# Kernel optimization log

Measured on AMD Instinct MI355X. Metric: run time of the kernel, lower is better.

Reference implementation:

```python
import jax, jax.numpy as jnp
import numpy as np

DIM = 1024
H = 16
D = DIM // H  # 64
EPS = 1e-6


def _rmsnorm(x, scale):
    # per-last-dim RMSNorm, computed in fp32 like the torch code
    rms = jax.lax.rsqrt(jnp.mean(x * x, axis=-1, keepdims=True) + EPS)
    return x * rms * scale


def _apply_rope(xq, xk, pe):
    # xq, xk: [B,H,L,D]; pe: [1,1,L,D/2,2,2]
    B, h, L, d = xq.shape
    xq_ = xq.reshape(B, h, L, d // 2, 1, 2)
    xk_ = xk.reshape(B, h, L, d // 2, 1, 2)
    xq_out = pe[..., 0] * xq_[..., 0] + pe[..., 1] * xq_[..., 1]  # [B,H,L,D/2,2]
    xk_out = pe[..., 0] * xk_[..., 0] + pe[..., 1] * xk_[..., 1]
    return xq_out.reshape(B, h, L, d), xk_out.reshape(B, h, L, d)


def setup_inputs() -> dict:
    key = jax.random.key(0)
    ks = jax.random.split(key, 6)
    B, L = 2, 2048
    x = jax.random.normal(ks[0], (B, L, DIM), dtype=jnp.float32)
    pe = jax.random.normal(ks[1], (1, 1, L, D // 2, 2, 2), dtype=jnp.float32)
    qkv_w = jax.random.normal(ks[2], (3 * DIM, DIM), dtype=jnp.float32) * (DIM ** -0.5)
    q_scale = jnp.ones((D,), dtype=jnp.float32)
    k_scale = jnp.ones((D,), dtype=jnp.float32)
    proj_w = jax.random.normal(ks[3], (DIM, DIM), dtype=jnp.float32) * (DIM ** -0.5)
    proj_b = jnp.zeros((DIM,), dtype=jnp.float32)
    return {"x": x, "pe": pe, "qkv_w": qkv_w, "q_scale": q_scale,
            "k_scale": k_scale, "proj_w": proj_w, "proj_b": proj_b}


def reference(x, pe, qkv_w, q_scale, k_scale, proj_w, proj_b):
    B, L, _ = x.shape
    x_c = jnp.clip(jnp.nan_to_num(x, nan=0.0, posinf=0.0, neginf=0.0), -10000.0, 10000.0)
    qkv = x_c @ qkv_w.T  # [B,L,3*DIM] (qkv_bias=False)
    qkv = jnp.nan_to_num(qkv, nan=0.0, posinf=0.0, neginf=0.0)
    # 'B L (K H D) -> K B H L D'
    qkv = qkv.reshape(B, L, 3, H, D).transpose(2, 0, 3, 1, 4)
    q, k, v = qkv[0], qkv[1], qkv[2]  # each [B,H,L,D]
    q = _rmsnorm(q, q_scale)
    k = _rmsnorm(k, k_scale)
    q, k = _apply_rope(q, k, pe)
    # scaled dot product attention (no mask)
    scores = jnp.einsum('bhqd,bhkd->bhqk', q, k) * (D ** -0.5)
    attn = jax.nn.softmax(scores, axis=-1)
    out = jnp.einsum('bhqk,bhkd->bhqd', attn, v)
    out = out.transpose(0, 2, 1, 3).reshape(B, L, H * D)  # 'B H L D -> B L (H D)'
    out = jnp.clip(out, -10000.0, 10000.0)
    return out @ proj_w.T + proj_b
```

## Files before the change

### kernel.cpp

```cpp
#include <hip/hip_runtime.h>
#include <hip/hip_bf16.h>

#define DIMC 1024
#define HEADS 16
#define HD 64
#define BATCH 2
#define SEQ 2048

typedef __bf16 bf16;
typedef __bf16 bf16x4 __attribute__((ext_vector_type(4)));
typedef __bf16 bf16x8 __attribute__((ext_vector_type(8)));
typedef float f32x4 __attribute__((ext_vector_type(4)));

typedef const __attribute__((address_space(1))) void* gas_t;
typedef __attribute__((address_space(3))) void* las_t;

__device__ inline f32x4 mfma_bf16(bf16x8 a, bf16x8 b, f32x4 c) {
    return __builtin_amdgcn_mfma_f32_16x16x32_bf16(a, b, c, 0, 0, 0);
}

__device__ inline void st8(bf16* p, bf16x8 v) {
    *(bf16x4*)p       = *(bf16x4*)&v;
    *(bf16x4*)(p + 4) = *((bf16x4*)&v + 1);
}
__device__ inline bf16x8 ld_frag(const bf16* p) {
    bf16x8 r;
    *(bf16x4*)&r       = *(const bf16x4*)p;
    *((bf16x4*)&r + 1) = *(const bf16x4*)(p + 16);
    return r;
}
__device__ inline bf16x8 ld_frag_s(const bf16* rowp, int cb, int sw) {
    bf16x8 r;
    *(bf16x4*)&r       = *(const bf16x4*)((const char*)rowp + ((cb) ^ sw));
    *((bf16x4*)&r + 1) = *(const bf16x4*)((const char*)rowp + ((cb + 32) ^ sw));
    return r;
}

__global__ __launch_bounds__(256) void k_prep_x(const float* __restrict__ x,
                                                bf16* __restrict__ xb) {
    int i = blockIdx.x * 256 + threadIdx.x;
    float4 v = ((const float4*)x)[i];
    float a[4] = {v.x, v.y, v.z, v.w};
    bf16x4 o;
#pragma unroll
    for (int j = 0; j < 4; ++j) {
        float f = a[j];
        f = __builtin_isfinite(f) ? fminf(fmaxf(f, -10000.f), 10000.f) : 0.f;
        o[j] = (bf16)f;
    }
    ((bf16x4*)xb)[i] = o;
}

__global__ __launch_bounds__(256) void k_cast(const float* __restrict__ a,
                                              bf16* __restrict__ o) {
    int i = blockIdx.x * 256 + threadIdx.x;
    float4 v = ((const float4*)a)[i];
    bf16x4 r = {(bf16)v.x, (bf16)v.y, (bf16)v.z, (bf16)v.w};
    ((bf16x4*)o)[i] = r;
}

template <bool OUT_BF16, bool BIAS, bool SANITIZE>
__global__ __launch_bounds__(256) void k_gemm_bt(const bf16* __restrict__ A,
                                                 const bf16* __restrict__ Bt,
                                                 void* __restrict__ Cv,
                                                 const float* __restrict__ bias,
                                                 int N, int K) {
    __shared__ alignas(16) bf16 As[128 * 64];
    __shared__ alignas(16) bf16 Bs[128 * 64];
    const int t = threadIdx.x;
    const int m0 = blockIdx.y * 128, n0 = blockIdx.x * 128;
    const int w = t >> 6, lane = t & 63;
    const int wm = (w >> 1) * 64, wn = (w & 1) * 64;
    const int lr = lane & 15, lg = lane >> 4;
    const int srow = lane >> 3;
    const int scol = ((lane & 7) ^ srow) * 8;
    const int sw = (lr & 7) << 4;

    f32x4 acc[4][4];
#pragma unroll
    for (int i = 0; i < 4; ++i)
#pragma unroll
        for (int j = 0; j < 4; ++j) acc[i][j] = 0.0f;

    for (int k0 = 0; k0 < K; k0 += 64) {
#pragma unroll
        for (int i = 0; i < 4; ++i) {
            int rg = w * 32 + i * 8;
            __builtin_amdgcn_global_load_lds(
                (gas_t)(A + (size_t)(m0 + rg + srow) * K + k0 + scol),
                (las_t)(As + rg * 64), 16, 0, 0);
            __builtin_amdgcn_global_load_lds(
                (gas_t)(Bt + (size_t)(n0 + rg + srow) * K + k0 + scol),
                (las_t)(Bs + rg * 64), 16, 0, 0);
        }
        __syncthreads();
#pragma unroll
        for (int kk = 0; kk < 2; ++kk) {
            const int cb = kk * 64 + lg * 8;
            bf16x8 af[4], bfr[4];
#pragma unroll
            for (int mi = 0; mi < 4; ++mi)
                af[mi] = ld_frag_s(&As[(wm + mi * 16 + lr) * 64], cb, sw);
#pragma unroll
            for (int ni = 0; ni < 4; ++ni)
                bfr[ni] = ld_frag_s(&Bs[(wn + ni * 16 + lr) * 64], cb, sw);
#pragma unroll
            for (int mi = 0; mi < 4; ++mi)
#pragma unroll
                for (int ni = 0; ni < 4; ++ni)
                    acc[mi][ni] = mfma_bf16(af[mi], bfr[ni], acc[mi][ni]);
        }
        __syncthreads();
    }
#pragma unroll
    for (int mi = 0; mi < 4; ++mi) {
#pragma unroll
        for (int ni = 0; ni < 4; ++ni) {
            int col = n0 + wn + ni * 16 + lr;
            float bval = BIAS ? bias[col] : 0.f;
#pragma unroll
            for (int r = 0; r < 4; ++r) {
                int row = m0 + wm + mi * 16 + lg * 4 + r;
                float v = acc[mi][ni][r];
                if (SANITIZE) v = __builtin_isfinite(v) ? v : 0.f;
                v += bval;
                if (OUT_BF16)
                    ((bf16*)Cv)[(size_t)row * N + col] = (bf16)v;
                else
                    ((float*)Cv)[(size_t)row * N + col] = v;
            }
        }
    }
}

__global__ __launch_bounds__(256) void k_post(const bf16* __restrict__ qkvb,
                                              const float* __restrict__ pe,
                                              const float* __restrict__ q_scale,
                                              const float* __restrict__ k_scale,
                                              bf16* __restrict__ qb,
                                              bf16* __restrict__ kb,
                                              bf16* __restrict__ vt) {
    const int lb = blockIdx.x, h = blockIdx.y, b = blockIdx.z;
    const int t = threadIdx.x;
    const int row = t >> 2, sub = t & 3;
    const int l = lb * 64 + row;
    const int d0 = sub * 16;
    const size_t rowbase = ((size_t)(b * SEQ + l)) * (3 * DIMC) + h * HD;
    const size_t bh = (size_t)(b * HEADS + h);

#pragma unroll
    for (int qk = 0; qk < 2; ++qk) {
        const bf16* src = qkvb + rowbase + qk * DIMC + d0;
        const float* sc = qk ? k_scale : q_scale;
        bf16x8 v0 = *(const bf16x8*)src;
        bf16x8 v1 = *(const bf16x8*)(src + 8);
        float vals[16];
        float ss = 0.f;
#pragma unroll
        for (int j = 0; j < 8; ++j) {
            vals[j] = (float)v0[j];
            vals[8 + j] = (float)v1[j];
        }
#pragma unroll
        for (int j = 0; j < 16; ++j) ss += vals[j] * vals[j];
        ss += __shfl_xor(ss, 1, 64);
        ss += __shfl_xor(ss, 2, 64);
        float rms = rsqrtf(ss * (1.f / 64.f) + 1e-6f);
        const float outscale = qk ? 1.0f : 0.125f * 1.44269504088896340736f;
        bf16 ob[16];
#pragma unroll
        for (int j = 0; j < 16; j += 2) {
            int d = d0 + j;
            float e0 = vals[j] * rms * sc[d];
            float e1 = vals[j + 1] * rms * sc[d + 1];
            float4 pv = *(const float4*)(pe + (size_t)l * 128 + (d >> 1) * 4);
            float o0 = pv.x * e0 + pv.y * e1;
            float o1 = pv.z * e0 + pv.w * e1;
            ob[j] = (bf16)(o0 * outscale);
            ob[j + 1] = (bf16)(o1 * outscale);
        }
        bf16* dst = (qk ? kb : qb) + (bh * SEQ + l) * HD + d0;
        *(bf16x8*)dst = *(bf16x8*)&ob[0];
        *(bf16x8*)(dst + 8) = *(bf16x8*)&ob[8];
    }

    __shared__ bf16 vlds[64][68];
    {
        const bf16* src = qkvb + rowbase + 2 * DIMC + d0;
        bf16x8 v0 = *(const bf16x8*)src;
        bf16x8 v1 = *(const bf16x8*)(src + 8);
        st8(&vlds[row][d0], v0);
        st8(&vlds[row][d0 + 8], v1);
    }
    __syncthreads();
    {
        const int d = t >> 2, c0 = (t & 3) * 16;
        bf16 ob[16];
#pragma unroll
        for (int j = 0; j < 16; ++j) ob[j] = vlds[c0 + j][d];
        bf16* dst = vt + (bh * HD + d) * SEQ + lb * 64 + c0;
        *(bf16x8*)dst = *(bf16x8*)&ob[0];
        *(bf16x8*)(dst + 8) = *(bf16x8*)&ob[8];
    }
}

__global__ __launch_bounds__(512) void k_attn(const bf16* __restrict__ Q,
                                              const bf16* __restrict__ Kb,
                                              const bf16* __restrict__ Vt,
                                              bf16* __restrict__ O) {
    __shared__ bf16 Ks[2][64][68];
    __shared__ bf16 Vs[2][64][68];
    const int qt = blockIdx.x, bh = blockIdx.y;
    const int b = bh >> 4, h = bh & 15;
    const int t = threadIdx.x, w = t >> 6, lane = t & 63;
    const int lr = lane & 15, lg = lane >> 4;
    const size_t baseQK = (size_t)bh * SEQ * HD;
    const size_t baseVt = (size_t)bh * HD * SEQ;

    const bf16* qp = Q + baseQK + (size_t)(qt * 128 + w * 16 + lr) * HD;
    bf16x8 qf0 = ld_frag(qp + lg * 4);
    bf16x8 qf1 = ld_frag(qp + 32 + lg * 4);

    const int sr = t >> 3, scol = (t & 7) * 8;
    {
        bf16x8 kv = *(const bf16x8*)(Kb + baseQK + (size_t)sr * HD + scol);
        bf16x8 vv = *(const bf16x8*)(Vt + baseVt + (size_t)sr * SEQ + scol);
        st8(&Ks[0][sr][scol], kv);
        st8(&Vs[0][sr][scol], vv);
    }
    __syncthreads();

    bf16x8 ones;
#pragma unroll
    for (int j = 0; j < 8; ++j) ones[j] = (bf16)1.0f;

    f32x4 oacc[4];
#pragma unroll
    for (int i = 0; i < 4; ++i) oacc[i] = 0.0f;
    f32x4 lacc = 0.0f;
    float m_s = -1e30f;

    int cur = 0;
    for (int kt = 0; kt < SEQ / 64; ++kt) {
        bf16x8 kreg, vreg;
        const bool pf = (kt + 1) < SEQ / 64;
        if (pf) {
            kreg = *(const bf16x8*)(Kb + baseQK + (size_t)((kt + 1) * 64 + sr) * HD + scol);
            vreg = *(const bf16x8*)(Vt + baseVt + (size_t)sr * SEQ + (kt + 1) * 64 + scol);
        }
        __builtin_amdgcn_s_setprio(1);
        f32x4 s[4];
#pragma unroll
        for (int nk = 0; nk < 4; ++nk) {
            f32x4 a = 0.0f;
            a = mfma_bf16(ld_frag(&Ks[cur][nk * 16 + lr][lg * 4]), qf0, a);
            a = mfma_bf16(ld_frag(&Ks[cur][nk * 16 + lr][32 + lg * 4]), qf1, a);
            s[nk] = a;
        }
        __builtin_amdgcn_s_setprio(0);
        float tm = fmaxf(fmaxf(s[0][0], s[0][1]), fmaxf(s[0][2], s[0][3]));
#pragma unroll
        for (int nk = 1; nk < 4; ++nk)
            tm = fmaxf(tm, fmaxf(fmaxf(s[nk][0], s[nk][1]),
                                 fmaxf(s[nk][2], s[nk][3])));
        tm = fmaxf(tm, __shfl_xor(tm, 16, 64));
        tm = fmaxf(tm, __shfl_xor(tm, 32, 64));
        if (!__all(tm <= m_s + 8.f)) {
            float mnew = fmaxf(m_s, tm);
            float alpha = exp2f(m_s - mnew);
            m_s = mnew;
#pragma unroll
            for (int nd = 0; nd < 4; ++nd)
#pragma unroll
                for (int r2 = 0; r2 < 4; ++r2) oacc[nd][r2] *= alpha;
#pragma unroll
            for (int r2 = 0; r2 < 4; ++r2) lacc[r2] *= alpha;
        }
        bf16x8 pa0, pa1;
#pragma unroll
        for (int j = 0; j < 4; ++j) {
            pa0[j]     = (bf16)exp2f(s[0][j] - m_s);
            pa0[4 + j] = (bf16)exp2f(s[1][j] - m_s);
            pa1[j]     = (bf16)exp2f(s[2][j] - m_s);
            pa1[4 + j] = (bf16)exp2f(s[3][j] - m_s);
        }
        __builtin_amdgcn_s_setprio(1);
        lacc = mfma_bf16(ones, pa0, lacc);
        lacc = mfma_bf16(ones, pa1, lacc);
#pragma unroll
        for (int nd = 0; nd < 4; ++nd) {
            oacc[nd] = mfma_bf16(ld_frag(&Vs[cur][nd * 16 + lr][lg * 4]), pa0, oacc[nd]);
            oacc[nd] = mfma_bf16(ld_frag(&Vs[cur][nd * 16 + lr][32 + lg * 4]), pa1, oacc[nd]);
        }
        __builtin_amdgcn_s_setprio(0);
        if (pf) {
            st8(&Ks[cur ^ 1][sr][scol], kreg);
            st8(&Vs[cur ^ 1][sr][scol], vreg);
        }
        __syncthreads();
        cur ^= 1;
    }
    {
        float inv = 1.f / lacc[0];
        int q = qt * 128 + w * 16 + lr;
#pragma unroll
        for (int nd = 0; nd < 4; ++nd) {
            bf16x4 ov;
#pragma unroll
            for (int r2 = 0; r2 < 4; ++r2) {
                float v = oacc[nd][r2] * inv;
                v = fminf(fmaxf(v, -10000.f), 10000.f);
                ov[r2] = (bf16)v;
            }
            *(bf16x4*)(O + ((size_t)(b * SEQ + q)) * DIMC + h * HD + nd * 16 + lg * 4) = ov;
        }
    }
}

extern "C" void kernel_launch(void* const* d_in, const int* in_sizes, int n_in,
                              void* d_out, int out_size, void* d_ws, size_t ws_size,
                              hipStream_t stream) {
    const float* x = (const float*)d_in[0];
    const float* pe = (const float*)d_in[1];
    const float* qkv_w = (const float*)d_in[2];
    const float* q_scale = (const float*)d_in[3];
    const float* k_scale = (const float*)d_in[4];
    const float* proj_w = (const float*)d_in[5];
    const float* proj_b = (const float*)d_in[6];
    float* out = (float*)d_out;
    char* ws = (char*)d_ws;

    bf16* xb = (bf16*)(ws);
    bf16* wqkv = (bf16*)(ws + (8u << 20));
    bf16* wproj = (bf16*)(ws + (14u << 20));
    bf16* qkvb = (bf16*)(ws + (16u << 20));
    bf16* ao = (bf16*)(ws + (16u << 20));
    bf16* qb = (bf16*)(ws + (40u << 20));
    bf16* kb = (bf16*)(ws + (48u << 20));
    bf16* vt = (bf16*)(ws + (56u << 20));

    k_prep_x<<<4096, 256, 0, stream>>>(x, xb);
    k_cast<<<3072, 256, 0, stream>>>(qkv_w, wqkv);
    k_cast<<<1024, 256, 0, stream>>>(proj_w, wproj);
    k_gemm_bt<true, false, true>
        <<<dim3(24, 32), 256, 0, stream>>>(xb, wqkv, (void*)qkvb, nullptr, 3072, 1024);
    k_post<<<dim3(32, HEADS, BATCH), 256, 0, stream>>>(qkvb, pe, q_scale, k_scale, qb, kb, vt);
    k_attn<<<dim3(SEQ / 128, BATCH * HEADS), 512, 0, stream>>>(qb, kb, vt, ao);
    k_gemm_bt<false, true, false>
        <<<dim3(8, 32), 256, 0, stream>>>(ao, wproj, (void*)out, proj_b, 1024, 1024);
}
```

Measured before the change: 156.2 us.

## Split attention KV range across wave halves and merge partial softmax states

The attention kernel now gives each block 64 queries instead of 128. Its eight waves form two halves, each covering half of the key/value sequence for the same 64 queries, and the two partial (max, sum, output) states are merged through shared memory at the end. This doubles the grid to 1024 blocks to improve occupancy and load balance across CUs, and a min-waves launch bound is added. In exchange, double buffering of K/V tiles is dropped in favour of a single buffer with an extra barrier per iteration, and each query's Q fragments are loaded twice.

```diff
diff --git a/kernel.cpp b/kernel.cpp
--- a/kernel.cpp
+++ b/kernel.cpp
@@ -204,29 +204,40 @@
     }
 }
 
-__global__ __launch_bounds__(512) void k_attn(const bf16* __restrict__ Q,
-                                              const bf16* __restrict__ Kb,
-                                              const bf16* __restrict__ Vt,
-                                              bf16* __restrict__ O) {
-    __shared__ bf16 Ks[2][64][68];
-    __shared__ bf16 Vs[2][64][68];
+__global__ __launch_bounds__(512, 6) void k_attn(const bf16* __restrict__ Q,
+                                                 const bf16* __restrict__ Kb,
+                                                 const bf16* __restrict__ Vt,
+                                                 bf16* __restrict__ O) {
+    __shared__ alignas(16) bf16 smem[4 * 64 * 68];
     const int qt = blockIdx.x, bh = blockIdx.y;
     const int b = bh >> 4, h = bh & 15;
     const int t = threadIdx.x, w = t >> 6, lane = t & 63;
     const int lr = lane & 15, lg = lane >> 4;
+    const int wq = w & 3;
+    const int half = w >> 2;
     const size_t baseQK = (size_t)bh * SEQ * HD;
     const size_t baseVt = (size_t)bh * HD * SEQ;
-
-    const bf16* qp = Q + baseQK + (size_t)(qt * 128 + w * 16 + lr) * HD;
+    const int NT = SEQ / 2 / 64;
+
+    bf16* Kmy = smem + half * 4352;
+    bf16* Vmy = smem + 8704 + half * 4352;
+
+    const bf16* qp = Q + baseQK + (size_t)(qt * 64 + wq * 16 + lr) * HD;
     bf16x8 qf0 = ld_frag(qp + lg * 4);
     bf16x8 qf1 = ld_frag(qp + 32 + lg * 4);
 
     const int sr = t >> 3, scol = (t & 7) * 8;
+    const bf16* kg0 = Kb + baseQK + (size_t)sr * HD + scol;
+    const bf16* vg0 = Vt + baseVt + (size_t)sr * SEQ + scol;
     {
-        bf16x8 kv = *(const bf16x8*)(Kb + baseQK + (size_t)sr * HD + scol);
-        bf16x8 vv = *(const bf16x8*)(Vt + baseVt + (size_t)sr * SEQ + scol);
-        st8(&Ks[0][sr][scol], kv);
-        st8(&Vs[0][sr][scol], vv);
+        bf16x8 k0 = *(const bf16x8*)(kg0);
+        bf16x8 k1 = *(const bf16x8*)(kg0 + (size_t)(SEQ / 2) * HD);
+        bf16x8 v0 = *(const bf16x8*)(vg0);
+        bf16x8 v1 = *(const bf16x8*)(vg0 + SEQ / 2);
+        st8(smem + sr * 68 + scol, k0);
+        st8(smem + 4352 + sr * 68 + scol, k1);
+        st8(smem + 8704 + sr * 68 + scol, v0);
+        st8(smem + 13056 + sr * 68 + scol, v1);
     }
     __syncthreads();
 
@@ -240,21 +251,24 @@
     f32x4 lacc = 0.0f;
     float m_s = -1e30f;
 
-    int cur = 0;
-    for (int kt = 0; kt < SEQ / 64; ++kt) {
-        bf16x8 kreg, vreg;
-        const bool pf = (kt + 1) < SEQ / 64;
+    for (int kt = 0; kt < NT; ++kt) {
+        bf16x8 k0r, k1r, v0r, v1r;
+        const bool pf = (kt + 1) < NT;
         if (pf) {
-            kreg = *(const bf16x8*)(Kb + baseQK + (size_t)((kt + 1) * 64 + sr) * HD + scol);
-            vreg = *(const bf16x8*)(Vt + baseVt + (size_t)sr * SEQ + (kt + 1) * 64 + scol);
+            const bf16* kg = kg0 + (size_t)((kt + 1) * 64) * HD;
+            const bf16* vg = vg0 + (kt + 1) * 64;
+            k0r = *(const bf16x8*)(kg);
+            k1r = *(const bf16x8*)(kg + (size_t)(SEQ / 2) * HD);
+            v0r = *(const bf16x8*)(vg);
+            v1r = *(const bf16x8*)(vg + SEQ / 2);
         }
         __builtin_amdgcn_s_setprio(1);
         f32x4 s[4];
 #pragma unroll
         for (int nk = 0; nk < 4; ++nk) {
             f32x4 a = 0.0f;
-            a = mfma_bf16(ld_frag(&Ks[cur][nk * 16 + lr][lg * 4]), qf0, a);
-            a = mfma_bf16(ld_frag(&Ks[cur][nk * 16 + lr][32 + lg * 4]), qf1, a);
+            a = mfma_bf16(ld_frag(Kmy + (nk * 16 + lr) * 68 + lg * 4), qf0, a);
+            a = mfma_bf16(ld_frag(Kmy + (nk * 16 + lr) * 68 + 32 + lg * 4), qf1, a);
             s[nk] = a;
         }
         __builtin_amdgcn_s_setprio(0);
@@ -289,26 +303,44 @@
         lacc = mfma_bf16(ones, pa1, lacc);
 #pragma unroll
         for (int nd = 0; nd < 4; ++nd) {
-            oacc[nd] = mfma_bf16(ld_frag(&Vs[cur][nd * 16 + lr][lg * 4]), pa0, oacc[nd]);
-            oacc[nd] = mfma_bf16(ld_frag(&Vs[cur][nd * 16 + lr][32 + lg * 4]), pa1, oacc[nd]);
+            oacc[nd] = mfma_bf16(ld_frag(Vmy + (nd * 16 + lr) * 68 + lg * 4), pa0, oacc[nd]);
+            oacc[nd] = mfma_bf16(ld_frag(Vmy + (nd * 16 + lr) * 68 + 32 + lg * 4), pa1, oacc[nd]);
         }
         __builtin_amdgcn_s_setprio(0);
+        __syncthreads();
         if (pf) {
-            st8(&Ks[cur ^ 1][sr][scol], kreg);
-            st8(&Vs[cur ^ 1][sr][scol], vreg);
-        }
-        __syncthreads();
-        cur ^= 1;
-    }
-    {
-        float inv = 1.f / lacc[0];
-        int q = qt * 128 + w * 16 + lr;
+            st8(smem + sr * 68 + scol, k0r);
+            st8(smem + 4352 + sr * 68 + scol, k1r);
+            st8(smem + 8704 + sr * 68 + scol, v0r);
+            st8(smem + 13056 + sr * 68 + scol, v1r);
+            __syncthreads();
+        }
+    }
+    float* xf = (float*)smem;
+    if (w >= 4) {
+        int slot = ((w - 4) * 64 + lane) * 18;
+#pragma unroll
+        for (int nd = 0; nd < 4; ++nd)
+#pragma unroll
+            for (int r2 = 0; r2 < 4; ++r2) xf[slot + nd * 4 + r2] = oacc[nd][r2];
+        xf[slot + 16] = m_s;
+        xf[slot + 17] = lacc[0];
+    }
+    __syncthreads();
+    if (w < 4) {
+        int slot = (w * 64 + lane) * 18;
+        float m_b = xf[slot + 16], l_b = xf[slot + 17];
+        float m_n = fmaxf(m_s, m_b);
+        float aa = exp2f(m_s - m_n), ab = exp2f(m_b - m_n);
+        float l_n = lacc[0] * aa + l_b * ab;
+        float inv = 1.f / l_n;
+        int q = qt * 64 + wq * 16 + lr;
 #pragma unroll
         for (int nd = 0; nd < 4; ++nd) {
             bf16x4 ov;
 #pragma unroll
             for (int r2 = 0; r2 < 4; ++r2) {
-                float v = oacc[nd][r2] * inv;
+                float v = (oacc[nd][r2] * aa + xf[slot + nd * 4 + r2] * ab) * inv;
                 v = fminf(fmaxf(v, -10000.f), 10000.f);
                 ov[r2] = (bf16)v;
             }
@@ -345,7 +377,7 @@
     k_gemm_bt<true, false, true>
         <<<dim3(24, 32), 256, 0, stream>>>(xb, wqkv, (void*)qkvb, nullptr, 3072, 1024);
     k_post<<<dim3(32, HEADS, BATCH), 256, 0, stream>>>(qkvb, pe, q_scale, k_scale, qb, kb, vt);
-    k_attn<<<dim3(SEQ / 128, BATCH * HEADS), 512, 0, stream>>>(qb, kb, vt, ao);
+    k_attn<<<dim3(SEQ / 64, BATCH * HEADS), 512, 0, stream>>>(qb, kb, vt, ao);
     k_gemm_bt<false, true, false>
         <<<dim3(8, 32), 256, 0, stream>>>(ao, wproj, (void*)out, proj_b, 1024, 1024);
 }
```

New measurement: 161.9 us. 3.7% more time.

## Fuse QKV RMSNorm/RoPE/V-transpose into GEMM epilogue and merge prep kernels

Applied to the files above, without the earlier changes.

Moves the per-head RMSNorm, RoPE, softmax prescale and V transpose into a dedicated QKV GEMM epilogue. Each 64-column warp tile maps to exactly one head, so the row reduction is done with lane shuffles. This removes the bf16 qkv intermediate round trip and a separate launch. The three cast/prep kernels are merged into one launch with 4 elements per thread. The epilogue now does scattered 2-byte stores for Q/K and strided 8-byte stores for V^T, which may coalesce worse.

```diff
diff --git a/kernel.cpp b/kernel.cpp
--- a/kernel.cpp
+++ b/kernel.cpp
@@ -36,27 +36,38 @@
     return r;
 }
 
-__global__ __launch_bounds__(256) void k_prep_x(const float* __restrict__ x,
-                                                bf16* __restrict__ xb) {
-    int i = blockIdx.x * 256 + threadIdx.x;
-    float4 v = ((const float4*)x)[i];
-    float a[4] = {v.x, v.y, v.z, v.w};
-    bf16x4 o;
-#pragma unroll
-    for (int j = 0; j < 4; ++j) {
-        float f = a[j];
-        f = __builtin_isfinite(f) ? fminf(fmaxf(f, -10000.f), 10000.f) : 0.f;
-        o[j] = (bf16)f;
-    }
-    ((bf16x4*)xb)[i] = o;
-}
-
-__global__ __launch_bounds__(256) void k_cast(const float* __restrict__ a,
-                                              bf16* __restrict__ o) {
-    int i = blockIdx.x * 256 + threadIdx.x;
-    float4 v = ((const float4*)a)[i];
-    bf16x4 r = {(bf16)v.x, (bf16)v.y, (bf16)v.z, (bf16)v.w};
-    ((bf16x4*)o)[i] = r;
+__global__ __launch_bounds__(256) void k_prep_all(const float* __restrict__ x,
+                                                  const float* __restrict__ qw,
+                                                  const float* __restrict__ pw,
+                                                  bf16* __restrict__ xb,
+                                                  bf16* __restrict__ wqkv,
+                                                  bf16* __restrict__ wproj) {
+    int idx = blockIdx.x * 1024 + threadIdx.x;
+#pragma unroll
+    for (int j = 0; j < 4; ++j, idx += 256) {
+        if (idx < 1048576) {
+            float4 v = ((const float4*)x)[idx];
+            float a[4] = {v.x, v.y, v.z, v.w};
+            bf16x4 o;
+#pragma unroll
+            for (int q = 0; q < 4; ++q) {
+                float f = a[q];
+                f = __builtin_isfinite(f) ? fminf(fmaxf(f, -10000.f), 10000.f) : 0.f;
+                o[q] = (bf16)f;
+            }
+            ((bf16x4*)xb)[idx] = o;
+        } else if (idx < 1835008) {
+            int i2 = idx - 1048576;
+            float4 v = ((const float4*)qw)[i2];
+            bf16x4 o = {(bf16)v.x, (bf16)v.y, (bf16)v.z, (bf16)v.w};
+            ((bf16x4*)wqkv)[i2] = o;
+        } else {
+            int i2 = idx - 1835008;
+            float4 v = ((const float4*)pw)[i2];
+            bf16x4 o = {(bf16)v.x, (bf16)v.y, (bf16)v.z, (bf16)v.w};
+            ((bf16x4*)wproj)[i2] = o;
+        }
+    }
 }
 
 template <bool OUT_BF16, bool BIAS, bool SANITIZE>
@@ -133,74 +144,125 @@
     }
 }
 
-__global__ __launch_bounds__(256) void k_post(const bf16* __restrict__ qkvb,
-                                              const float* __restrict__ pe,
-                                              const float* __restrict__ q_scale,
-                                              const float* __restrict__ k_scale,
-                                              bf16* __restrict__ qb,
-                                              bf16* __restrict__ kb,
-                                              bf16* __restrict__ vt) {
-    const int lb = blockIdx.x, h = blockIdx.y, b = blockIdx.z;
-    const int t = threadIdx.x;
-    const int row = t >> 2, sub = t & 3;
-    const int l = lb * 64 + row;
-    const int d0 = sub * 16;
-    const size_t rowbase = ((size_t)(b * SEQ + l)) * (3 * DIMC) + h * HD;
-    const size_t bh = (size_t)(b * HEADS + h);
-
-#pragma unroll
-    for (int qk = 0; qk < 2; ++qk) {
-        const bf16* src = qkvb + rowbase + qk * DIMC + d0;
-        const float* sc = qk ? k_scale : q_scale;
-        bf16x8 v0 = *(const bf16x8*)src;
-        bf16x8 v1 = *(const bf16x8*)(src + 8);
-        float vals[16];
-        float ss = 0.f;
-#pragma unroll
-        for (int j = 0; j < 8; ++j) {
-            vals[j] = (float)v0[j];
-            vals[8 + j] = (float)v1[j];
-        }
-#pragma unroll
-        for (int j = 0; j < 16; ++j) ss += vals[j] * vals[j];
-        ss += __shfl_xor(ss, 1, 64);
-        ss += __shfl_xor(ss, 2, 64);
-        float rms = rsqrtf(ss * (1.f / 64.f) + 1e-6f);
-        const float outscale = qk ? 1.0f : 0.125f * 1.44269504088896340736f;
-        bf16 ob[16];
-#pragma unroll
-        for (int j = 0; j < 16; j += 2) {
-            int d = d0 + j;
-            float e0 = vals[j] * rms * sc[d];
-            float e1 = vals[j + 1] * rms * sc[d + 1];
-            float4 pv = *(const float4*)(pe + (size_t)l * 128 + (d >> 1) * 4);
-            float o0 = pv.x * e0 + pv.y * e1;
-            float o1 = pv.z * e0 + pv.w * e1;
-            ob[j] = (bf16)(o0 * outscale);
-            ob[j + 1] = (bf16)(o1 * outscale);
-        }
-        bf16* dst = (qk ? kb : qb) + (bh * SEQ + l) * HD + d0;
-        *(bf16x8*)dst = *(bf16x8*)&ob[0];
-        *(bf16x8*)(dst + 8) = *(bf16x8*)&ob[8];
-    }
-
-    __shared__ bf16 vlds[64][68];
-    {
-        const bf16* src = qkvb + rowbase + 2 * DIMC + d0;
-        bf16x8 v0 = *(const bf16x8*)src;
-        bf16x8 v1 = *(const bf16x8*)(src + 8);
-        st8(&vlds[row][d0], v0);
-        st8(&vlds[row][d0 + 8], v1);
-    }
-    __syncthreads();
-    {
-        const int d = t >> 2, c0 = (t & 3) * 16;
-        bf16 ob[16];
-#pragma unroll
-        for (int j = 0; j < 16; ++j) ob[j] = vlds[c0 + j][d];
-        bf16* dst = vt + (bh * HD + d) * SEQ + lb * 64 + c0;
-        *(bf16x8*)dst = *(bf16x8*)&ob[0];
-        *(bf16x8*)(dst + 8) = *(bf16x8*)&ob[8];
+__global__ __launch_bounds__(256) void k_gemm_qkv(const bf16* __restrict__ A,
+                                                  const bf16* __restrict__ Bt,
+                                                  const float* __restrict__ pe,
+                                                  const float* __restrict__ q_scale,
+                                                  const float* __restrict__ k_scale,
+                                                  bf16* __restrict__ qb,
+                                                  bf16* __restrict__ kb,
+                                                  bf16* __restrict__ vt) {
+    __shared__ alignas(16) bf16 As[128 * 64];
+    __shared__ alignas(16) bf16 Bs[128 * 64];
+    const int K = DIMC, t = threadIdx.x;
+    const int m0 = blockIdx.y * 128, n0 = blockIdx.x * 128;
+    const int w = t >> 6, lane = t & 63;
+    const int wm = (w >> 1) * 64, wn = (w & 1) * 64;
+    const int lr = lane & 15, lg = lane >> 4;
+    const int srow = lane >> 3;
+    const int scol = ((lane & 7) ^ srow) * 8;
+    const int sw = (lr & 7) << 4;
+
+    f32x4 acc[4][4];
+#pragma unroll
+    for (int i = 0; i < 4; ++i)
+#pragma unroll
+        for (int j = 0; j < 4; ++j) acc[i][j] = 0.0f;
+
+    for (int k0 = 0; k0 < K; k0 += 64) {
+#pragma unroll
+        for (int i = 0; i < 4; ++i) {
+            int rg = w * 32 + i * 8;
+            __builtin_amdgcn_global_load_lds(
+                (gas_t)(A + (size_t)(m0 + rg + srow) * K + k0 + scol),
+                (las_t)(As + rg * 64), 16, 0, 0);
+            __builtin_amdgcn_global_load_lds(
+                (gas_t)(Bt + (size_t)(n0 + rg + srow) * K + k0 + scol),
+                (las_t)(Bs + rg * 64), 16, 0, 0);
+        }
+        __syncthreads();
+#pragma unroll
+        for (int kk = 0; kk < 2; ++kk) {
+            const int cb = kk * 64 + lg * 8;
+            bf16x8 af[4], bfr[4];
+#pragma unroll
+            for (int mi = 0; mi < 4; ++mi)
+                af[mi] = ld_frag_s(&As[(wm + mi * 16 + lr) * 64], cb, sw);
+#pragma unroll
+            for (int ni = 0; ni < 4; ++ni)
+                bfr[ni] = ld_frag_s(&Bs[(wn + ni * 16 + lr) * 64], cb, sw);
+#pragma unroll
+            for (int mi = 0; mi < 4; ++mi)
+#pragma unroll
+                for (int ni = 0; ni < 4; ++ni)
+                    acc[mi][ni] = mfma_bf16(af[mi], bfr[ni], acc[mi][ni]);
+        }
+        __syncthreads();
+    }
+
+    const int g = (n0 + wn) >> 6;
+    const int sel = g >> 4;
+    const int hh = g & 15;
+    const int row0 = m0 + wm;
+    const int bb = row0 >> 11;
+    const int l0 = row0 & (SEQ - 1);
+    const size_t bhh = (size_t)(bb * HEADS + hh);
+
+#pragma unroll
+    for (int mi = 0; mi < 4; ++mi)
+#pragma unroll
+        for (int ni = 0; ni < 4; ++ni)
+#pragma unroll
+            for (int r = 0; r < 4; ++r) {
+                float v = acc[mi][ni][r];
+                acc[mi][ni][r] = __builtin_isfinite(v) ? v : 0.f;
+            }
+
+    if (sel == 2) {
+#pragma unroll
+        for (int mi = 0; mi < 4; ++mi)
+#pragma unroll
+            for (int ni = 0; ni < 4; ++ni) {
+                bf16x4 ov;
+#pragma unroll
+                for (int r = 0; r < 4; ++r) ov[r] = (bf16)acc[mi][ni][r];
+                *(bf16x4*)(vt + (bhh * HD + ni * 16 + lr) * SEQ +
+                           l0 + mi * 16 + lg * 4) = ov;
+            }
+    } else {
+        const float* sc = sel ? k_scale : q_scale;
+        bf16* dst = sel ? kb : qb;
+        const float oscale = sel ? 1.0f : 0.125f * 1.44269504088896340736f;
+        float scv[4];
+#pragma unroll
+        for (int ni = 0; ni < 4; ++ni) scv[ni] = sc[ni * 16 + lr];
+#pragma unroll
+        for (int mi = 0; mi < 4; ++mi) {
+#pragma unroll
+            for (int r = 0; r < 4; ++r) {
+                float ss = 0.f;
+#pragma unroll
+                for (int ni = 0; ni < 4; ++ni)
+                    ss += acc[mi][ni][r] * acc[mi][ni][r];
+                ss += __shfl_xor(ss, 1, 64);
+                ss += __shfl_xor(ss, 2, 64);
+                ss += __shfl_xor(ss, 4, 64);
+                ss += __shfl_xor(ss, 8, 64);
+                float rms = rsqrtf(ss * (1.f / 64.f) + 1e-6f);
+                int l = l0 + mi * 16 + lg * 4 + r;
+                const float* peb = pe + (size_t)l * 128 + (lr & 1) * 2;
+                bf16* db = dst + (bhh * SEQ + l) * HD + lr;
+#pragma unroll
+                for (int ni = 0; ni < 4; ++ni) {
+                    float e = acc[mi][ni][r] * rms * scv[ni];
+                    float p = __shfl_xor(e, 1, 64);
+                    float2 pv = *(const float2*)(peb + (ni * 8 + (lr >> 1)) * 4);
+                    float ee = (lr & 1) ? p : e;
+                    float eo = (lr & 1) ? e : p;
+                    db[ni * 16] = (bf16)((pv.x * ee + pv.y * eo) * oscale);
+                }
+            }
+        }
     }
 }
 
@@ -333,18 +395,14 @@
     bf16* xb = (bf16*)(ws);
     bf16* wqkv = (bf16*)(ws + (8u << 20));
     bf16* wproj = (bf16*)(ws + (14u << 20));
-    bf16* qkvb = (bf16*)(ws + (16u << 20));
     bf16* ao = (bf16*)(ws + (16u << 20));
-    bf16* qb = (bf16*)(ws + (40u << 20));
-    bf16* kb = (bf16*)(ws + (48u << 20));
-    bf16* vt = (bf16*)(ws + (56u << 20));
-
-    k_prep_x<<<4096, 256, 0, stream>>>(x, xb);
-    k_cast<<<3072, 256, 0, stream>>>(qkv_w, wqkv);
-    k_cast<<<1024, 256, 0, stream>>>(proj_w, wproj);
-    k_gemm_bt<true, false, true>
-        <<<dim3(24, 32), 256, 0, stream>>>(xb, wqkv, (void*)qkvb, nullptr, 3072, 1024);
-    k_post<<<dim3(32, HEADS, BATCH), 256, 0, stream>>>(qkvb, pe, q_scale, k_scale, qb, kb, vt);
+    bf16* qb = (bf16*)(ws + (24u << 20));
+    bf16* kb = (bf16*)(ws + (32u << 20));
+    bf16* vt = (bf16*)(ws + (40u << 20));
+
+    k_prep_all<<<2048, 256, 0, stream>>>(x, qkv_w, proj_w, xb, wqkv, wproj);
+    k_gemm_qkv<<<dim3(24, 32), 256, 0, stream>>>(xb, wqkv, pe, q_scale, k_scale,
+                                                 qb, kb, vt);
     k_attn<<<dim3(SEQ / 128, BATCH * HEADS), 512, 0, stream>>>(qb, kb, vt, ao);
     k_gemm_bt<false, true, false>
         <<<dim3(8, 32), 256, 0, stream>>>(ao, wproj, (void*)out, proj_b, 1024, 1024);
```

Result: no change. 155.0 us (-0.8%).
